# Kernel optimization log

Measured on AMD Instinct MI355X. Metric: run time of the kernel, lower is better.

## Reference

```python
import jax, jax.numpy as jnp
import numpy as np

B, L, S, C, H = 2, 2048, 2048, 1024, 16
HD = C // H  # head_dim = 64


def setup_inputs() -> dict:
    key = jax.random.key(0)
    k0, k1, k2, k3, k4 = jax.random.split(key, 5)
    w_scale = 1.0 / np.sqrt(C).astype(np.float32)
    return {
        "x0": jax.random.normal(k0, (B, L, C), jnp.float32),
        "x1": jax.random.normal(k1, (B, S, C), jnp.float32),
        "Wqk": jax.random.normal(k2, (C, C), jnp.float32) * w_scale,
        "Wv": jax.random.normal(k3, (C, C), jnp.float32) * w_scale,
        "Wmerge": jax.random.normal(k4, (C, C), jnp.float32) * w_scale,
    }


def reference(x0, x1, Wqk, Wv, Wmerge):
    softmax_temp = HD ** -0.5
    scale = softmax_temp ** 0.5  # applied to both qk0 and qk1

    def split_heads(t):  # [B,N,C] -> [B,N,H,HD]
        return t.reshape(t.shape[0], t.shape[1], H, HD)

    # shared QK projection (same weight for both streams), torch Linear: y = x @ W^T
    qk0 = split_heads(x0 @ Wqk.T) * scale  # [B,L,H,HD]
    qk1 = split_heads(x1 @ Wqk.T) * scale  # [B,S,H,HD]
    v0 = split_heads(x0 @ Wv.T)            # [B,L,H,HD]
    v1 = split_heads(x1 @ Wv.T)            # [B,S,H,HD]

    # single similarity matrix reused for both softmax directions
    sim = jnp.einsum('blhd,bshd->bhls', qk0, qk1)  # [B,H,L,S]
    attn01 = jax.nn.softmax(sim, axis=-1)  # softmax over S (x0 attends x1)
    attn10 = jax.nn.softmax(sim, axis=-2)  # softmax over L (== softmax(sim^T, -1))

    o0 = jnp.einsum('bhls,bshd->blhd', attn01, v1).reshape(x0.shape[0], x0.shape[1], C)
    o1 = jnp.einsum('bhls,blhd->bshd', attn10, v0).reshape(x1.shape[0], x1.shape[1], C)

    return (o0 @ Wmerge.T, o1 @ Wmerge.T)
```

## Files before the change

kernel.cpp:

```cpp
#include <hip/hip_runtime.h>
#include <hip/hip_bf16.h>
#include <stdint.h>


typedef __attribute__((ext_vector_type(8))) short bf16x8;
typedef __attribute__((ext_vector_type(4))) float f32x4;
typedef __attribute__((ext_vector_type(16))) float f32x16;
typedef __attribute__((ext_vector_type(4))) unsigned int u32x4;
typedef __attribute__((ext_vector_type(2))) unsigned int u32x2;
typedef __bf16 bf16_2 __attribute__((ext_vector_type(2)));

typedef const __attribute__((address_space(1))) unsigned int gu32;
typedef __attribute__((address_space(3))) unsigned int lu32;

__device__ __forceinline__ unsigned short f2bf(float f) {
  unsigned int u = __builtin_bit_cast(unsigned int, f);
  u += 0x7fffu + ((u >> 16) & 1u);
  return (unsigned short)(u >> 16);
}

__device__ __forceinline__ unsigned int cvtpk(float lo, float hi_) {
  bf16_2 t = { (__bf16)lo, (__bf16)hi_ };
  return __builtin_bit_cast(unsigned int, t);
}

__device__ __forceinline__ unsigned short f2bf_hw(float f) {
  return __builtin_bit_cast(unsigned short, (__bf16)f);
}

__global__ void cvt_x(const float* __restrict__ x0, const float* __restrict__ x1,
                      unsigned short* __restrict__ dst) {
  const long NX = 4194304;
  int y = blockIdx.y;
  const float* src = y ? x1 : x0;
  long i = ((long)blockIdx.x * 256 + threadIdx.x) * 8;
  float4 a = *(const float4*)(src + i);
  float4 b = *(const float4*)(src + i + 4);
  union { unsigned short u[8]; bf16x8 v; } r;
  r.u[0] = f2bf(a.x); r.u[1] = f2bf(a.y); r.u[2] = f2bf(a.z); r.u[3] = f2bf(a.w);
  r.u[4] = f2bf(b.x); r.u[5] = f2bf(b.y); r.u[6] = f2bf(b.z); r.u[7] = f2bf(b.w);
  *(bf16x8*)(dst + y * NX + i) = r.v;
}

__global__ void cvt_w(const float* __restrict__ w0, const float* __restrict__ w1,
                      const float* __restrict__ w2, unsigned short* __restrict__ dst) {
  const long NW = 1048576;
  int y = blockIdx.y;
  const float* src = (y == 0) ? w0 : ((y == 1) ? w1 : w2);
  long i = ((long)blockIdx.x * 256 + threadIdx.x) * 8;
  float4 a = *(const float4*)(src + i);
  float4 b = *(const float4*)(src + i + 4);
  union { unsigned short u[8]; bf16x8 v; } r;
  r.u[0] = f2bf(a.x); r.u[1] = f2bf(a.y); r.u[2] = f2bf(a.z); r.u[3] = f2bf(a.w);
  r.u[4] = f2bf(b.x); r.u[5] = f2bf(b.y); r.u[6] = f2bf(b.z); r.u[7] = f2bf(b.w);
  *(bf16x8*)(dst + y * NW + i) = r.v;
}

template<int OUTF32>
__global__ __launch_bounds__(256, 2)
void gemm_bt(const unsigned short* __restrict__ A, const unsigned short* __restrict__ B,
             void* __restrict__ C, int M, int N, int K, float scale) {
  __shared__ unsigned short As[128 * 32];
  __shared__ unsigned short Bs[128 * 32];
  const int tid = threadIdx.x;
  const int lane = tid & 63, w = tid >> 6;
  const int il = lane & 15, g = lane >> 4;
  const int wr = w >> 1, wc = w & 1;
  const int bm = blockIdx.y * 128, bn = blockIdx.x * 128;
  f32x4 acc[4][4];
#pragma unroll
  for (int m = 0; m < 4; ++m)
#pragma unroll
    for (int n = 0; n < 4; ++n) acc[m][n] = (f32x4){0.f, 0.f, 0.f, 0.f};

  const int crow = lane >> 2, ccol = (lane & 3) * 8;
  const int ch0 = w * 2, ch1 = w * 2 + 1;
  const unsigned short* pa0 = A + (long)(bm + ch0 * 16 + crow) * K + ccol;
  const unsigned short* pa1 = A + (long)(bm + ch1 * 16 + crow) * K + ccol;
  const unsigned short* pb0 = B + (long)(bn + ch0 * 16 + crow) * K + ccol;
  const unsigned short* pb1 = B + (long)(bn + ch1 * 16 + crow) * K + ccol;

  for (int k0 = 0; k0 < K; k0 += 32) {
    __builtin_amdgcn_global_load_lds((gu32*)(pa0 + k0), (lu32*)(As + ch0 * 512), 16, 0, 0);
    __builtin_amdgcn_global_load_lds((gu32*)(pa1 + k0), (lu32*)(As + ch1 * 512), 16, 0, 0);
    __builtin_amdgcn_global_load_lds((gu32*)(pb0 + k0), (lu32*)(Bs + ch0 * 512), 16, 0, 0);
    __builtin_amdgcn_global_load_lds((gu32*)(pb1 + k0), (lu32*)(Bs + ch1 * 512), 16, 0, 0);
    __syncthreads();
    bf16x8 av[4], bv[4];
#pragma unroll
    for (int m = 0; m < 4; ++m)
      av[m] = *(const bf16x8*)(As + (wr * 64 + m * 16 + il) * 32 + g * 8);
#pragma unroll
    for (int n = 0; n < 4; ++n)
      bv[n] = *(const bf16x8*)(Bs + (wc * 64 + n * 16 + il) * 32 + g * 8);
#pragma unroll
    for (int m = 0; m < 4; ++m)
#pragma unroll
      for (int n = 0; n < 4; ++n)
        acc[m][n] = __builtin_amdgcn_mfma_f32_16x16x32_bf16(av[m], bv[n], acc[m][n], 0, 0, 0);
    __syncthreads();
  }

#pragma unroll
  for (int m = 0; m < 4; ++m) {
    long row0 = bm + wr * 64 + m * 16 + g * 4;
#pragma unroll
    for (int n = 0; n < 4; ++n) {
      long col = bn + wc * 64 + n * 16 + il;
#pragma unroll
      for (int r = 0; r < 4; ++r) {
        float v = acc[m][n][r] * scale;
        if (OUTF32) ((float*)C)[(row0 + r) * (long)N + col] = v;
        else        ((unsigned short*)C)[(row0 + r) * (long)N + col] = f2bf(v);
      }
    }
  }
}

__global__ __launch_bounds__(256, 2)
void gemm_qkv(const unsigned short* __restrict__ A, const unsigned short* __restrict__ B,
              unsigned short* __restrict__ C0, unsigned short* __restrict__ vt, float scale0) {
  __shared__ unsigned short As[128 * 32];
  __shared__ unsigned short Bs[128 * 32];
  __shared__ unsigned short T[128][136];
  const int K = 1024;
  const int tid = threadIdx.x;
  const int lane = tid & 63, w = tid >> 6;
  const int il = lane & 15, g = lane >> 4;
  const int wr = w >> 1, wc = w & 1;
  const int bm = blockIdx.y * 128, bnn = blockIdx.x * 128;
  f32x4 acc[4][4];
#pragma unroll
  for (int m = 0; m < 4; ++m)
#pragma unroll
    for (int n = 0; n < 4; ++n) acc[m][n] = (f32x4){0.f, 0.f, 0.f, 0.f};

  const int crow = lane >> 2, ccol = (lane & 3) * 8;
  const int ch0 = w * 2, ch1 = w * 2 + 1;
  const unsigned short* pa0 = A + (long)(bm + ch0 * 16 + crow) * K + ccol;
  const unsigned short* pa1 = A + (long)(bm + ch1 * 16 + crow) * K + ccol;
  const unsigned short* pb0 = B + (long)(bnn + ch0 * 16 + crow) * K + ccol;
  const unsigned short* pb1 = B + (long)(bnn + ch1 * 16 + crow) * K + ccol;

  for (int k0 = 0; k0 < K; k0 += 32) {
    __builtin_amdgcn_global_load_lds((gu32*)(pa0 + k0), (lu32*)(As + ch0 * 512), 16, 0, 0);
    __builtin_amdgcn_global_load_lds((gu32*)(pa1 + k0), (lu32*)(As + ch1 * 512), 16, 0, 0);
    __builtin_amdgcn_global_load_lds((gu32*)(pb0 + k0), (lu32*)(Bs + ch0 * 512), 16, 0, 0);
    __builtin_amdgcn_global_load_lds((gu32*)(pb1 + k0), (lu32*)(Bs + ch1 * 512), 16, 0, 0);
    __syncthreads();
    bf16x8 av[4], bv[4];
#pragma unroll
    for (int m = 0; m < 4; ++m)
      av[m] = *(const bf16x8*)(As + (wr * 64 + m * 16 + il) * 32 + g * 8);
#pragma unroll
    for (int n = 0; n < 4; ++n)
      bv[n] = *(const bf16x8*)(Bs + (wc * 64 + n * 16 + il) * 32 + g * 8);
#pragma unroll
    for (int m = 0; m < 4; ++m)
#pragma unroll
      for (int n = 0; n < 4; ++n)
        acc[m][n] = __builtin_amdgcn_mfma_f32_16x16x32_bf16(av[m], bv[n], acc[m][n], 0, 0, 0);
    __syncthreads();
  }

  if (bnn < 1024) {
#pragma unroll
    for (int m = 0; m < 4; ++m) {
      long row0 = bm + wr * 64 + m * 16 + g * 4;
#pragma unroll
      for (int n = 0; n < 4; ++n) {
        long col = bnn + wc * 64 + n * 16 + il;
#pragma unroll
        for (int r = 0; r < 4; ++r)
          C0[(row0 + r) * 1024 + col] = f2bf(acc[m][n][r] * scale0);
      }
    }
  } else {
#pragma unroll
    for (int m = 0; m < 4; ++m) {
      int rl = wr * 64 + m * 16 + g * 4;
#pragma unroll
      for (int n = 0; n < 4; ++n) {
        int cl = wc * 64 + n * 16 + il;
        u32x2 pk = { cvtpk(acc[m][n][0], acc[m][n][1]), cvtpk(acc[m][n][2], acc[m][n][3]) };
        *(u32x2*)&T[cl][rl] = pk;
      }
    }
    __syncthreads();
    int cl2 = tid & 127, half = tid >> 7;
    int s = bm >> 11;
    int h0 = (bnn - 1024) >> 6;
    unsigned short* dst = vt + (((long)(s * 16 + h0 + (cl2 >> 6))) * 64 + (cl2 & 63)) * 2048
                             + (bm & 2047) + half * 64;
#pragma unroll
    for (int j = 0; j < 8; ++j)
      *(bf16x8*)(dst + j * 8) = *(const bf16x8*)&T[cl2][half * 64 + j * 8];
  }
}

__global__ __launch_bounds__(256, 4)
void attn_kernel(const unsigned short* __restrict__ qk,
                 const unsigned short* __restrict__ vt,
                 unsigned short* __restrict__ o) {
  __shared__ unsigned short sK[2][4096];
  __shared__ unsigned short sV[2][4096];
  int bid = blockIdx.x;
  int lb = (bid & 7) * 128 + (bid >> 3);
  int tid = threadIdx.x;
  int w = tid >> 6, lane = tid & 63;
  int u = lb * 4 + w;
  int dir = u >> 11, bh = (u >> 6) & 31, qu = u & 63;
  int b = bh >> 4, h = bh & 15;
  int q = lane & 31, hi = lane >> 5;

  long qrow0 = (dir ? 4096L : 0L) + b * 2048L + (long)qu * 32L;
  long krow0 = (dir ? 0L : 4096L) + b * 2048L;
  int vs = dir ? b : 2 + b;
  long vrow0 = (long)(vs * 16 + h) * 64;

  const unsigned short* Qp = qk + (qrow0 + q) * 1024 + h * 64 + hi * 8;

  int srow = tid >> 3;
  int sc = ((tid & 7) * 8) ^ ((srow & 7) << 3);
  const unsigned short* kg = qk + (krow0 + srow) * 1024 + h * 64 + sc;
  const unsigned short* vg = vt + (vrow0 + srow) * 2048 + sc;
  const int wbase = w * 512;

#define STAGE(BUF, T)                                                                    \
  {                                                                                      \
    long jj = (long)(T) * 64;                                                            \
    __builtin_amdgcn_global_load_lds((gu32*)(kg + jj * 1024),        (lu32*)(sK[BUF] + wbase),        16, 0, 0); \
    __builtin_amdgcn_global_load_lds((gu32*)(kg + (jj + 32) * 1024), (lu32*)(sK[BUF] + wbase + 2048), 16, 0, 0); \
    __builtin_amdgcn_global_load_lds((gu32*)(vg + jj),               (lu32*)(sV[BUF] + wbase),        16, 0, 0); \
    __builtin_amdgcn_global_load_lds((gu32*)(vg + jj + 32 * 2048),   (lu32*)(sV[BUF] + wbase + 2048), 16, 0, 0); \
  }

  bf16x8 qf[4];
#pragma unroll
  for (int ds = 0; ds < 4; ++ds)
    qf[ds] = *(const bf16x8*)(Qp + ds * 16);

  f32x16 z16;
#pragma unroll
  for (int j = 0; j < 16; ++j) z16[j] = 0.f;
  f32x16 accO[2];
  accO[0] = z16; accO[1] = z16;
  f32x16 lsum = z16;
  const short oneb = (short)0x3F80;
  const bf16x8 ones = {oneb, oneb, oneb, oneb, oneb, oneb, oneb, oneb};

  STAGE(0, 0);
  __syncthreads();

#pragma unroll 1
  for (int t = 0; t < 32; ++t) {
    int cur = t & 1;
    if (t < 31) STAGE(cur ^ 1, t + 1);

    bf16x8 kf[8], vf[8];
    int cswz = (q & 7) << 3;
#pragma unroll
    for (int kb = 0; kb < 2; ++kb)
#pragma unroll
      for (int ds = 0; ds < 4; ++ds)
        kf[kb * 4 + ds] = *(const bf16x8*)(&sK[cur][(kb * 32 + q) * 64 + ((ds * 16 + hi * 8) ^ cswz)]);
#pragma unroll
    for (int ks = 0; ks < 4; ++ks)
#pragma unroll
      for (int dn = 0; dn < 2; ++dn)
        vf[ks * 2 + dn] = *(const bf16x8*)(&sV[cur][(dn * 32 + q) * 64 + ((ks * 16 + hi * 8) ^ cswz)]);

    f32x16 st0 = __builtin_amdgcn_mfma_f32_32x32x16_bf16(kf[0], qf[0], z16, 0, 0, 0);
    f32x16 st1 = __builtin_amdgcn_mfma_f32_32x32x16_bf16(kf[4], qf[0], z16, 0, 0, 0);
#pragma unroll
    for (int ds = 1; ds < 4; ++ds)
      st0 = __builtin_amdgcn_mfma_f32_32x32x16_bf16(kf[ds], qf[ds], st0, 0, 0, 0);
#pragma unroll
    for (int ds = 1; ds < 4; ++ds)
      st1 = __builtin_amdgcn_mfma_f32_32x32x16_bf16(kf[4 + ds], qf[ds], st1, 0, 0, 0);

#pragma unroll
    for (int j = 0; j < 16; ++j) {
      st0[j] = __builtin_amdgcn_exp2f(st0[j]);
      st1[j] = __builtin_amdgcn_exp2f(st1[j]);
    }

    bf16x8 pa[4];
#pragma unroll
    for (int ks = 0; ks < 4; ++ks) {
      int m0 = (ks & 1) * 8;
      unsigned int a0, a1, b0, b1;
      if (ks < 2) {
        a0 = cvtpk(st0[m0],     st0[m0 + 1]); a1 = cvtpk(st0[m0 + 2], st0[m0 + 3]);
        b0 = cvtpk(st0[m0 + 4], st0[m0 + 5]); b1 = cvtpk(st0[m0 + 6], st0[m0 + 7]);
      } else {
        a0 = cvtpk(st1[m0],     st1[m0 + 1]); a1 = cvtpk(st1[m0 + 2], st1[m0 + 3]);
        b0 = cvtpk(st1[m0 + 4], st1[m0 + 5]); b1 = cvtpk(st1[m0 + 6], st1[m0 + 7]);
      }
      u32x2 r0 = __builtin_amdgcn_permlane32_swap(a0, b0, false, false);
      u32x2 r1 = __builtin_amdgcn_permlane32_swap(a1, b1, false, false);
      u32x4 uu = {r0[0], r1[0], r0[1], r1[1]};
      pa[ks] = __builtin_bit_cast(bf16x8, uu);
    }
#pragma unroll
    for (int ks = 0; ks < 4; ++ks)
      lsum = __builtin_amdgcn_mfma_f32_32x32x16_bf16(pa[ks], ones, lsum, 0, 0, 0);
#pragma unroll
    for (int ks = 0; ks < 4; ++ks)
#pragma unroll
      for (int dn = 0; dn < 2; ++dn)
        accO[dn] = __builtin_amdgcn_mfma_f32_32x32x16_bf16(pa[ks], vf[ks * 2 + dn], accO[dn], 0, 0, 0);

    __syncthreads();
  }
#undef STAGE

#pragma unroll
  for (int r = 0; r < 16; ++r) {
    int row = (r & 3) + 8 * (r >> 2) + 4 * hi;
    float invr = 1.f / lsum[r];
    long orow = qrow0 + row;
#pragma unroll
    for (int dn = 0; dn < 2; ++dn)
      o[orow * 1024 + h * 64 + dn * 32 + q] = f2bf_hw(accO[dn][r] * invr);
  }
}

extern "C" void kernel_launch(void* const* d_in, const int* in_sizes, int n_in,
                              void* d_out, int out_size, void* d_ws, size_t ws_size,
                              hipStream_t stream) {
  const float* x0 = (const float*)d_in[0];
  const float* x1 = (const float*)d_in[1];
  const float* Wqk = (const float*)d_in[2];
  const float* Wv = (const float*)d_in[3];
  const float* Wm = (const float*)d_in[4];
  float* out = (float*)d_out;

  const long NX = 4194304;
  const long NW = 1048576;
  unsigned short* xb  = (unsigned short*)d_ws;
  unsigned short* wb  = xb + 2 * NX;
  unsigned short* qkb = wb + 3 * NW;
  unsigned short* vb  = qkb + 2 * NX;
  unsigned short* vtb = vb + 2 * NX;

  cvt_x<<<dim3(2048, 2), 256, 0, stream>>>(x0, x1, xb);
  cvt_w<<<dim3(512, 3), 256, 0, stream>>>(Wqk, Wv, Wm, wb);

  const float sqk = 0.35355339059327373f * 1.2011224087864498f;
  gemm_qkv<<<dim3(16, 64), 256, 0, stream>>>(xb, wb, qkb, vtb, sqk);
  attn_kernel<<<1024, 256, 0, stream>>>(qkb, vtb, vb);
  gemm_bt<1><<<dim3(8, 64), 256, 0, stream>>>(vb, wb + 2 * NW, out, 8192, 1024, 1024, 1.f);
}
```

Baseline: 173.4 us.

## Rewrite QKV GEMM as 256x256 tile, 8-wave kernel with multi-stage LDS pipeline

Replaces the 128x128, 4-wave, single-buffered QKV projection GEMM with a 256x256 tile, 8-wave kernel. It uses 128 KB of dynamic LDS, double buffered and split into half-tiles, with XOR-swizzled layout. Global-to-LDS loads for later k-steps are interleaved with MFMA compute on the current half-tiles, using explicit vmcnt waits and barriers, so load latency is hidden and data reuse per block rises. The V transpose epilogue is done in two passes through the shared buffer. The risks are lower occupancy, fewer blocks (256) across the CUs, and fragile hand-scheduled wait counts.

```diff
diff --git a/kernel.cpp b/kernel.cpp
--- a/kernel.cpp
+++ b/kernel.cpp
@@ -117,56 +117,100 @@
   }
 }
 
-__global__ __launch_bounds__(256, 2)
-void gemm_qkv(const unsigned short* __restrict__ A, const unsigned short* __restrict__ B,
-              unsigned short* __restrict__ C0, unsigned short* __restrict__ vt, float scale0) {
-  __shared__ unsigned short As[128 * 32];
-  __shared__ unsigned short Bs[128 * 32];
-  __shared__ unsigned short T[128][136];
-  const int K = 1024;
+
+#define QSTAGEA(BUF, MH, TT)                                                              \
+  {                                                                                       \
+    long kc = (long)(TT) * 64 + sslot * 8;                                                \
+    const unsigned short* s0 = Ag + (long)(bm + (MH) * 64 + srow) * 1024 + kc;            \
+    const unsigned short* s1 = Ag + (long)(bm + 128 + (MH) * 64 + srow) * 1024 + kc;      \
+    __builtin_amdgcn_global_load_lds((gu32*)s0, (lu32*)(smem + ((BUF)*2+(MH))*8192 + dbase), 16, 0, 0);        \
+    __builtin_amdgcn_global_load_lds((gu32*)s1, (lu32*)(smem + ((BUF)*2+(MH))*8192 + 4096 + dbase), 16, 0, 0); \
+  }
+
+#define QSTAGEB(BUF, NH, TT)                                                              \
+  {                                                                                       \
+    long kc = (long)(TT) * 64 + sslot * 8;                                                \
+    const unsigned short* s0 = Bg + (long)(bnn + ((srow >> 5) * 64) + (NH) * 32 + (srow & 31)) * 1024 + kc;        \
+    const unsigned short* s1 = Bg + (long)(bnn + (((64 + srow) >> 5) * 64) + (NH) * 32 + (srow & 31)) * 1024 + kc; \
+    __builtin_amdgcn_global_load_lds((gu32*)s0, (lu32*)(smem + 32768 + ((BUF)*2+(NH))*8192 + dbase), 16, 0, 0);        \
+    __builtin_amdgcn_global_load_lds((gu32*)s1, (lu32*)(smem + 32768 + ((BUF)*2+(NH))*8192 + 4096 + dbase), 16, 0, 0); \
+  }
+
+#define QCOMPUTE(RBUF, MH, NH)                                                            \
+  {                                                                                       \
+    const unsigned short* Ar = smem + ((RBUF)*2+(MH))*8192 + (wr * 64 + il) * 64;         \
+    const unsigned short* Br = smem + 32768 + ((RBUF)*2+(NH))*8192 + (wc * 32 + il) * 64; \
+    bf16x8 av[4][2], bv[2][2];                                                            \
+    _Pragma("unroll")                                                                     \
+    for (int mp = 0; mp < 4; ++mp)                                                        \
+      _Pragma("unroll")                                                                   \
+      for (int ks = 0; ks < 2; ++ks)                                                      \
+        av[mp][ks] = *(const bf16x8*)(Ar + mp * 1024 + (((ks * 4 + g) ^ sw) * 8));        \
+    _Pragma("unroll")                                                                     \
+    for (int np = 0; np < 2; ++np)                                                        \
+      _Pragma("unroll")                                                                   \
+      for (int ks = 0; ks < 2; ++ks)                                                      \
+        bv[np][ks] = *(const bf16x8*)(Br + np * 1024 + (((ks * 4 + g) ^ sw) * 8));        \
+    _Pragma("unroll")                                                                     \
+    for (int mp = 0; mp < 4; ++mp)                                                        \
+      _Pragma("unroll")                                                                   \
+      for (int np = 0; np < 2; ++np) {                                                    \
+        acc[(MH)*4+mp][(NH)*2+np] = __builtin_amdgcn_mfma_f32_16x16x32_bf16(av[mp][0], bv[np][0], acc[(MH)*4+mp][(NH)*2+np], 0, 0, 0); \
+        acc[(MH)*4+mp][(NH)*2+np] = __builtin_amdgcn_mfma_f32_16x16x32_bf16(av[mp][1], bv[np][1], acc[(MH)*4+mp][(NH)*2+np], 0, 0, 0); \
+      }                                                                                   \
+  }
+
+#define QEND(W4)                                                                          \
+  {                                                                                       \
+    if (W4) asm volatile("s_waitcnt vmcnt(4)" ::: "memory");                              \
+    asm volatile("" ::: "memory");                                                        \
+    __builtin_amdgcn_s_barrier();                                                         \
+    asm volatile("" ::: "memory");                                                        \
+  }
+
+__global__ __launch_bounds__(512, 2)
+void gemm_qkv8(const unsigned short* __restrict__ Ag, const unsigned short* __restrict__ Bg,
+               unsigned short* __restrict__ C0, unsigned short* __restrict__ vt, float scale0) {
+  extern __shared__ unsigned short smem[];
   const int tid = threadIdx.x;
-  const int lane = tid & 63, w = tid >> 6;
+  const int lane = tid & 63, wid = tid >> 6;
   const int il = lane & 15, g = lane >> 4;
-  const int wr = w >> 1, wc = w & 1;
-  const int bm = blockIdx.y * 128, bnn = blockIdx.x * 128;
-  f32x4 acc[4][4];
-#pragma unroll
-  for (int m = 0; m < 4; ++m)
+  const int wr = wid >> 2, wc = wid & 3;
+  const int sw = il & 7;
+  const int bm = blockIdx.y * 256, bnn = blockIdx.x * 256;
+
+  const int srow = tid >> 3;
+  const int sslot = (tid & 7) ^ ((tid >> 3) & 7);
+  const int dbase = (tid >> 6) * 512;
+
+  f32x4 acc[8][4];
+#pragma unroll
+  for (int m = 0; m < 8; ++m)
 #pragma unroll
     for (int n = 0; n < 4; ++n) acc[m][n] = (f32x4){0.f, 0.f, 0.f, 0.f};
 
-  const int crow = lane >> 2, ccol = (lane & 3) * 8;
-  const int ch0 = w * 2, ch1 = w * 2 + 1;
-  const unsigned short* pa0 = A + (long)(bm + ch0 * 16 + crow) * K + ccol;
-  const unsigned short* pa1 = A + (long)(bm + ch1 * 16 + crow) * K + ccol;
-  const unsigned short* pb0 = B + (long)(bnn + ch0 * 16 + crow) * K + ccol;
-  const unsigned short* pb1 = B + (long)(bnn + ch1 * 16 + crow) * K + ccol;
-
-  for (int k0 = 0; k0 < K; k0 += 32) {
-    __builtin_amdgcn_global_load_lds((gu32*)(pa0 + k0), (lu32*)(As + ch0 * 512), 16, 0, 0);
-    __builtin_amdgcn_global_load_lds((gu32*)(pa1 + k0), (lu32*)(As + ch1 * 512), 16, 0, 0);
-    __builtin_amdgcn_global_load_lds((gu32*)(pb0 + k0), (lu32*)(Bs + ch0 * 512), 16, 0, 0);
-    __builtin_amdgcn_global_load_lds((gu32*)(pb1 + k0), (lu32*)(Bs + ch1 * 512), 16, 0, 0);
-    __syncthreads();
-    bf16x8 av[4], bv[4];
-#pragma unroll
-    for (int m = 0; m < 4; ++m)
-      av[m] = *(const bf16x8*)(As + (wr * 64 + m * 16 + il) * 32 + g * 8);
-#pragma unroll
-    for (int n = 0; n < 4; ++n)
-      bv[n] = *(const bf16x8*)(Bs + (wc * 64 + n * 16 + il) * 32 + g * 8);
-#pragma unroll
-    for (int m = 0; m < 4; ++m)
-#pragma unroll
-      for (int n = 0; n < 4; ++n)
-        acc[m][n] = __builtin_amdgcn_mfma_f32_16x16x32_bf16(av[m], bv[n], acc[m][n], 0, 0, 0);
-    __syncthreads();
-  }
+  QSTAGEA(0, 0, 0); QSTAGEA(0, 1, 0); QSTAGEB(0, 0, 0); QSTAGEB(0, 1, 0);
+  QSTAGEB(1, 0, 1); QSTAGEA(1, 1, 1);
+  __syncthreads();
+
+#pragma unroll 1
+  for (int i = 0; i < 8; ++i) {
+    const int t1 = 2 * i + 1, t2 = (2 * i + 2) & 15, t3 = (2 * i + 3) & 15;
+    QSTAGEA(1, 0, t1); QCOMPUTE(0, 0, 0); QEND(0);
+    QSTAGEB(1, 1, t1); QCOMPUTE(0, 1, 0); QEND(0);
+    QSTAGEB(0, 0, t2); QCOMPUTE(0, 1, 1); QEND(0);
+    QSTAGEA(0, 1, t2); QCOMPUTE(0, 0, 1); QEND(1);
+    QSTAGEA(0, 0, t2); QCOMPUTE(1, 0, 0); QEND(0);
+    QSTAGEB(0, 1, t2); QCOMPUTE(1, 1, 0); QEND(0);
+    QSTAGEB(1, 0, t3); QCOMPUTE(1, 1, 1); QEND(0);
+    QSTAGEA(1, 1, t3); QCOMPUTE(1, 0, 1); QEND(1);
+  }
+  __syncthreads();
 
   if (bnn < 1024) {
 #pragma unroll
-    for (int m = 0; m < 4; ++m) {
-      long row0 = bm + wr * 64 + m * 16 + g * 4;
+    for (int m = 0; m < 8; ++m) {
+      long row0 = bm + wr * 128 + m * 16 + g * 4;
 #pragma unroll
       for (int n = 0; n < 4; ++n) {
         long col = bnn + wc * 64 + n * 16 + il;
@@ -176,25 +220,32 @@
       }
     }
   } else {
-#pragma unroll
-    for (int m = 0; m < 4; ++m) {
-      int rl = wr * 64 + m * 16 + g * 4;
-#pragma unroll
-      for (int n = 0; n < 4; ++n) {
-        int cl = wc * 64 + n * 16 + il;
-        u32x2 pk = { cvtpk(acc[m][n][0], acc[m][n][1]), cvtpk(acc[m][n][2], acc[m][n][3]) };
-        *(u32x2*)&T[cl][rl] = pk;
+    unsigned short (*T)[264] = (unsigned short (*)[264])smem;
+    const int s = bm >> 11;
+#pragma unroll 1
+    for (int p = 0; p < 2; ++p) {
+      if ((wc >> 1) == p) {
+#pragma unroll
+        for (int m = 0; m < 8; ++m) {
+          int rl = wr * 128 + m * 16 + g * 4;
+#pragma unroll
+          for (int n = 0; n < 4; ++n) {
+            int cl = (wc & 1) * 64 + n * 16 + il;
+            u32x2 pk = { cvtpk(acc[m][n][0], acc[m][n][1]), cvtpk(acc[m][n][2], acc[m][n][3]) };
+            *(u32x2*)&T[cl][rl] = pk;
+          }
+        }
       }
+      __syncthreads();
+      int cl2 = tid & 127, portion = tid >> 7;
+      int col = (bnn - 1024) + p * 128 + cl2;
+      unsigned short* dst = vt + (((long)(s * 16 + (col >> 6))) * 64 + (col & 63)) * 2048
+                               + (bm & 2047) + portion * 64;
+#pragma unroll
+      for (int j = 0; j < 8; ++j)
+        *(bf16x8*)(dst + j * 8) = *(const bf16x8*)&T[cl2][portion * 64 + j * 8];
+      __syncthreads();
     }
-    __syncthreads();
-    int cl2 = tid & 127, half = tid >> 7;
-    int s = bm >> 11;
-    int h0 = (bnn - 1024) >> 6;
-    unsigned short* dst = vt + (((long)(s * 16 + h0 + (cl2 >> 6))) * 64 + (cl2 & 63)) * 2048
-                             + (bm & 2047) + half * 64;
-#pragma unroll
-    for (int j = 0; j < 8; ++j)
-      *(bf16x8*)(dst + j * 8) = *(const bf16x8*)&T[cl2][half * 64 + j * 8];
   }
 }
 
@@ -348,7 +399,7 @@
   cvt_w<<<dim3(512, 3), 256, 0, stream>>>(Wqk, Wv, Wm, wb);
 
   const float sqk = 0.35355339059327373f * 1.2011224087864498f;
-  gemm_qkv<<<dim3(16, 64), 256, 0, stream>>>(xb, wb, qkb, vtb, sqk);
+  gemm_qkv8<<<dim3(8, 32), 512, 131072, stream>>>(xb, wb, qkb, vtb, sqk);
   attn_kernel<<<1024, 256, 0, stream>>>(qkb, vtb, vb);
   gemm_bt<1><<<dim3(8, 64), 256, 0, stream>>>(vb, wb + 2 * NW, out, 8192, 1024, 1024, 1.f);
 }
```

After: 161.8 us. 6.7% less time.
